# Kernel tuning notes

Hardware: AMD Instinct MI355X
Metric: run time of the kernel (lower is better)

The kernel has to match this reference:

```python
import jax, jax.numpy as jnp
import numpy as np

HEADS = 16
DIMS = [64, 64, 64, 64]  # [d_att(Q), d_att(K), d_ff(V), d_ff(G)]
EPS = 1e-4
P_POW = 2


def _cdist(Q, K):
    # Euclidean pairwise distance via the norm expansion, like torch.cdist.
    # Q: [h, b, t, d], K: [h, b, t, d] -> [h, b, t, t]
    q2 = jnp.sum(Q * Q, axis=-1)  # [h, b, t]
    k2 = jnp.sum(K * K, axis=-1)  # [h, b, t]
    qk = jnp.einsum('hbtd,hbsd->hbts', Q, K)
    d2 = q2[..., :, None] + k2[..., None, :] - 2.0 * qk
    return jnp.sqrt(jnp.maximum(d2, 0.0))


def setup_inputs() -> dict:
    key = jax.random.key(0)
    ks = jax.random.split(key, 4)
    b, t, d_in = 2, 2048, 1024
    d_proj = HEADS * sum(DIMS)  # 4096
    X = jax.random.normal(ks[0], (b, t, d_in), dtype=jnp.float32)
    W_in = jax.random.normal(ks[1], (d_in, d_proj), dtype=jnp.float32) * (d_in ** -0.5)
    b_in = jnp.zeros((d_proj,), dtype=jnp.float32)
    W_out = jax.random.normal(ks[2], (HEADS * DIMS[2], d_in), dtype=jnp.float32) * ((HEADS * DIMS[2]) ** -0.5)
    b_out = jnp.zeros((d_in,), dtype=jnp.float32)
    return {"X": X, "W_in": W_in, "b_in": b_in, "W_out": W_out, "b_out": b_out}


def reference(X, W_in, b_in, W_out, b_out):
    b, t, _ = X.shape
    # multi-head input projection: [b,t,d_in] -> [h,b,t,sum(DIMS)] -> split
    P = X @ W_in + b_in                       # [b, t, h*sum(DIMS)]
    P = P.reshape(b, t, HEADS, sum(DIMS))
    P = jnp.transpose(P, (2, 0, 1, 3))        # [h, b, t, sum(DIMS)]
    splits = np.cumsum(DIMS)[:-1]
    Q, K, V, G = jnp.split(P, splits, axis=-1)
    # Shepard's attention: inverse-power-distance weights
    W = jnp.power(EPS + _cdist(Q, K), -P_POW)         # [h, b, t, t]
    W = W / (EPS + jnp.sum(W, axis=-1, keepdims=True))
    A = jnp.einsum('hbts,hbse->hbte', W, V)           # [h, b, t, e]
    H = G * A                                          # gating
    H = jnp.transpose(H, (1, 2, 0, 3)).reshape(b, t, HEADS * DIMS[2])
    return H @ W_out + b_out
```

## Files before the change

### kernel.cpp

```cpp
#include <hip/hip_runtime.h>
#include <hip/hip_bf16.h>
#include <cstdint>
#include <cstddef>

typedef __bf16 bf16_t;
typedef __attribute__((ext_vector_type(8))) __bf16 bf16x8;
typedef __attribute__((ext_vector_type(4))) float f32x4;
typedef __attribute__((ext_vector_type(16))) float f32x16;
typedef __attribute__((ext_vector_type(4))) unsigned int u32x4;

#define ATT_EPS 1e-4f

__device__ __forceinline__ f32x4 mfma_bf16(bf16x8 a, bf16x8 b, f32x4 c) {
  return __builtin_amdgcn_mfma_f32_16x16x32_bf16(a, b, c, 0, 0, 0);
}
__device__ __forceinline__ f32x16 mfma32(bf16x8 a, bf16x8 b, f32x16 c) {
  return __builtin_amdgcn_mfma_f32_32x32x16_bf16(a, b, c, 0, 0, 0);
}
__device__ __forceinline__ unsigned cvtpk_bf16(float lo, float hi) {
  unsigned r;
  asm("v_cvt_pk_bf16_f32 %0, %1, %2" : "=v"(r) : "v"(lo), "v"(hi));
  return r;
}

#define GLDS16(g, l)                                                          \
  __builtin_amdgcn_global_load_lds(                                           \
      (const __attribute__((address_space(1))) void*)(g),                     \
      (__attribute__((address_space(3))) void*)(l), 16, 0, 0)

#define BARRAW() asm volatile("s_barrier" ::: "memory")
#define WAITVN(n) asm volatile("s_waitcnt vmcnt(" #n ")" ::: "memory")

__global__ __launch_bounds__(256) void prep_kernel(
    const float* __restrict__ Wi, bf16_t* __restrict__ WiT,
    const float* __restrict__ Wo, bf16_t* __restrict__ WoT,
    const float* __restrict__ X, bf16_t* __restrict__ Xb) {
  __shared__ float T[64][65];
  if (blockIdx.y >= 20) {
    int i = ((blockIdx.y - 20) * 64 + blockIdx.x) * 256 + threadIdx.x;
    const f32x4* src = (const f32x4*)X + (size_t)i * 4;
    f32x4 a = src[0], b = src[1], c = src[2], d = src[3];
    bf16x8 o0, o1;
    o0[0] = (__bf16)a[0]; o0[1] = (__bf16)a[1]; o0[2] = (__bf16)a[2]; o0[3] = (__bf16)a[3];
    o0[4] = (__bf16)b[0]; o0[5] = (__bf16)b[1]; o0[6] = (__bf16)b[2]; o0[7] = (__bf16)b[3];
    o1[0] = (__bf16)c[0]; o1[1] = (__bf16)c[1]; o1[2] = (__bf16)c[2]; o1[3] = (__bf16)c[3];
    o1[4] = (__bf16)d[0]; o1[5] = (__bf16)d[1]; o1[6] = (__bf16)d[2]; o1[7] = (__bf16)d[3];
    ((bf16x8*)Xb)[(size_t)i * 2] = o0;
    ((bf16x8*)Xb)[(size_t)i * 2 + 1] = o1;
    return;
  }
  int tx = threadIdx.x & 63, ty = threadIdx.x >> 6;
  const float* W;
  bf16_t* Wt;
  int c0, r0, R, C;
  if (blockIdx.y < 16) {
    W = Wi; Wt = WiT; R = 1024; C = 4096;
    c0 = blockIdx.x * 64; r0 = blockIdx.y * 64;
  } else {
    int idx = (blockIdx.y - 16) * 64 + blockIdx.x;
    if (idx >= 256) return;
    W = Wo; Wt = WoT; R = 1024; C = 1024;
    c0 = (idx & 15) * 64; r0 = (idx >> 4) * 64;
  }
#pragma unroll
  for (int i = 0; i < 16; ++i) {
    int rr = ty * 16 + i;
    T[rr][tx] = W[(size_t)(r0 + rr) * C + c0 + tx];
  }
  __syncthreads();
#pragma unroll
  for (int i = 0; i < 16; ++i) {
    int cc = ty * 16 + i;
    Wt[(size_t)(c0 + cc) * R + r0 + tx] = (bf16_t)T[tx][cc];
  }
}

__global__ __launch_bounds__(512, 2) void gemm1_kernel(
    const bf16_t* __restrict__ A, const bf16_t* __restrict__ Bt,
    const float* __restrict__ bias, bf16_t* __restrict__ P,
    float* __restrict__ Q2, bf16_t* __restrict__ K2E, bf16_t* __restrict__ VtG) {
  __shared__ bf16_t As[4][2][128 * 32];
  __shared__ bf16_t Bs[4][2][128 * 32];

  const int K = 1024, N = 4096;
  int tid = threadIdx.x, lane = tid & 63, wv = tid >> 6;
  int l15 = lane & 15, lhi = lane >> 4;
  int wm = wv >> 2, wn = wv & 3;
  int swz = (blockIdx.x & 7) * 32 + (blockIdx.x >> 3);
  int tm = swz >> 4, tn = swz & 15;
  int m0 = tm << 8, n0 = tn << 8;
  int h = tn;

  int srow = tid >> 2, su = tid & 3;
  int scc = (su ^ ((srow >> 1) & 3)) << 3;
  auto stage2 = [&](int t, int pq) {
    int k0 = t * 32 + scc;
    if (pq == 0) {
      GLDS16(A + (size_t)(m0 + srow) * K + k0, &As[t & 3][0][tid * 8]);
      GLDS16(A + (size_t)(m0 + 128 + srow) * K + k0, &As[t & 3][1][tid * 8]);
    } else {
      GLDS16(Bt + (size_t)(n0 + srow) * K + k0, &Bs[t & 3][0][tid * 8]);
      GLDS16(Bt + (size_t)(n0 + 128 + srow) * K + k0, &Bs[t & 3][1][tid * 8]);
    }
  };

  f32x4 zero = {0.f, 0.f, 0.f, 0.f};
  f32x4 acc[8][4];
#pragma unroll
  for (int mf = 0; mf < 8; ++mf)
#pragma unroll
    for (int nf = 0; nf < 4; ++nf) acc[mf][nf] = zero;

  int bh = wn >> 1;
  int cidb = (wn & 1) * 64 + l15;

  stage2(0, 0); stage2(0, 1);
  stage2(1, 0); stage2(1, 1);
  stage2(2, 0); stage2(2, 1);
  WAITVN(8);
  BARRAW();

  for (int t = 0; t < 32; ++t) {
    int buf = t & 3;
    bf16x8 af0[4], bfr[4];
#pragma unroll
    for (int i = 0; i < 4; ++i) {
      int mfr = i * 16 + l15;
      af0[i] = *(const bf16x8*)&As[buf][wm][mfr * 32 + ((lhi ^ ((mfr >> 1) & 3)) << 3)];
    }
#pragma unroll
    for (int nf = 0; nf < 4; ++nf) {
      int cid = cidb + nf * 16;
      bfr[nf] = *(const bf16x8*)&Bs[buf][bh][cid * 32 + ((lhi ^ ((cid >> 1) & 3)) << 3)];
    }
    if (t + 3 < 32) stage2(t + 3, 0);
#pragma unroll
    for (int i = 0; i < 4; ++i)
#pragma unroll
      for (int nf = 0; nf < 4; ++nf)
        acc[i][nf] = mfma_bf16(af0[i], bfr[nf], acc[i][nf]);
    bf16x8 af1[4];
#pragma unroll
    for (int i = 0; i < 4; ++i) {
      int mfr = (4 + i) * 16 + l15;
      af1[i] = *(const bf16x8*)&As[buf][wm][mfr * 32 + ((lhi ^ ((mfr >> 1) & 3)) << 3)];
    }
    if (t + 3 < 32) stage2(t + 3, 1);
#pragma unroll
    for (int i = 0; i < 4; ++i)
#pragma unroll
      for (int nf = 0; nf < 4; ++nf)
        acc[4 + i][nf] = mfma_bf16(af1[i], bfr[nf], acc[4 + i][nf]);
    if (t <= 28) WAITVN(8);
    else if (t == 29) WAITVN(4);
    else if (t == 30) WAITVN(0);
    BARRAW();
  }

#pragma unroll
  for (int nf = 0; nf < 4; ++nf) {
    float bv = bias[n0 + wn * 64 + nf * 16 + l15];
#pragma unroll
    for (int mf = 0; mf < 8; ++mf)
#pragma unroll
      for (int r = 0; r < 4; ++r) acc[mf][nf][r] += bv;
  }

  if (wn != 2) {
#pragma unroll
    for (int nf = 0; nf < 4; ++nf) {
      int col = n0 + wn * 64 + nf * 16 + l15;
#pragma unroll
      for (int mf = 0; mf < 8; ++mf) {
        int rowb = m0 + wm * 128 + mf * 16 + lhi * 4;
#pragma unroll
        for (int r = 0; r < 4; ++r)
          P[(size_t)(rowb + r) * N + col] = (bf16_t)acc[mf][nf][r];
      }
    }
  }

  if (wn < 2) {
#pragma unroll
    for (int mf = 0; mf < 8; ++mf)
#pragma unroll
      for (int r = 0; r < 4; ++r) {
        float s = 0.f;
#pragma unroll
        for (int nf = 0; nf < 4; ++nf) s += acc[mf][nf][r] * acc[mf][nf][r];
        s += __shfl_xor(s, 1);
        s += __shfl_xor(s, 2);
        s += __shfl_xor(s, 4);
        s += __shfl_xor(s, 8);
        if (l15 == 0) {
          int row = m0 + wm * 128 + mf * 16 + lhi * 4 + r;
          if (wn == 0) {
            Q2[h * 4096 + row] = s;
          } else {
            __bf16 kh = (__bf16)s;
            __bf16 kl = (__bf16)(s - (float)kh);
            bf16x8 rw;
            rw[0] = kh; rw[1] = kl;
            rw[2] = (__bf16)1.f; rw[3] = (__bf16)1.f;
            rw[4] = (__bf16)0.f; rw[5] = (__bf16)0.f;
            rw[6] = (__bf16)0.f; rw[7] = (__bf16)0.f;
            *(bf16x8*)&K2E[((size_t)h * 4096 + row) * 8] = rw;
          }
        }
      }
  }

  bf16_t* T = &As[0][0][0];
  if (wn == 2) {
#pragma unroll
    for (int mf = 0; mf < 8; ++mf)
#pragma unroll
      for (int nf = 0; nf < 4; ++nf)
#pragma unroll
        for (int r = 0; r < 4; ++r) {
          int row = wm * 128 + mf * 16 + lhi * 4 + r;
          int e = nf * 16 + l15;
          int prow = (row & ~15) | ((row & 3) | ((row & 4) << 1) | ((row & 8) >> 1));
          T[e * 264 + prow] = (bf16_t)acc[mf][nf][r];
        }
  }
  __syncthreads();
  {
    int e = tid >> 3, c0 = (tid & 7) * 32;
    bf16_t* dst = VtG + (size_t)(h * 64 + e) * 4096 + m0 + c0;
#pragma unroll
    for (int j = 0; j < 4; ++j)
      *(bf16x8*)&dst[j * 8] = *(bf16x8*)&T[e * 264 + c0 + j * 8];
  }
}

template <int OUTF32>
__global__ __launch_bounds__(256, 2) void gemm_kernel(
    const bf16_t* __restrict__ A, const bf16_t* __restrict__ Bt,
    const float* __restrict__ bias, void* __restrict__ Cout,
    int M, int N, int K) {
  __shared__ bf16_t As[2][128 * 64];
  __shared__ bf16_t Bs[2][128 * 64];
  int tid = threadIdx.x, lane = tid & 63, wv = tid >> 6;
  int l15 = lane & 15, lhi = lane >> 4;
  int NT = N >> 7;
  int nwg = gridDim.x;
  int qq = nwg >> 3;
  int swz = (blockIdx.x & 7) * qq + (blockIdx.x >> 3);
  int tm = swz / NT, tn = swz % NT;
  int m0 = tm << 7, n0 = tn << 7;
  int wm = (wv >> 1) << 6, wn = (wv & 1) << 6;
  int KT = K >> 6;

  auto stage = [&](int buf, int kt) {
    int k0 = kt << 6;
#pragma unroll
    for (int s = 0; s < 4; ++s) {
      int t = s * 256 + tid;
      int row = t >> 3, u = t & 7;
      int cc = (u ^ (row & 7)) << 3;
      GLDS16(A + (size_t)(m0 + row) * K + k0 + cc, &As[buf][t * 8]);
    }
#pragma unroll
    for (int s = 0; s < 4; ++s) {
      int t = s * 256 + tid;
      int row = t >> 3, u = t & 7;
      int cc = (u ^ (row & 7)) << 3;
      GLDS16(Bt + (size_t)(n0 + row) * K + k0 + cc, &Bs[buf][t * 8]);
    }
  };

  f32x4 zero = {0.f, 0.f, 0.f, 0.f};
  f32x4 acc[4][4];
#pragma unroll
  for (int ms = 0; ms < 4; ++ms)
#pragma unroll
    for (int ns = 0; ns < 4; ++ns) acc[ms][ns] = zero;

  stage(0, 0);
  __syncthreads();
  int cur = 0;
  for (int kt = 0; kt < KT; ++kt) {
    if (kt + 1 < KT) stage(cur ^ 1, kt + 1);
#pragma unroll
    for (int ks = 0; ks < 2; ++ks) {
      bf16x8 af[4], bfr[4];
#pragma unroll
      for (int ms = 0; ms < 4; ++ms) {
        int row = wm + ms * 16 + l15;
        af[ms] = *(const bf16x8*)&As[cur][row * 64 + (((ks * 4 + lhi) ^ (row & 7)) << 3)];
      }
#pragma unroll
      for (int ns = 0; ns < 4; ++ns) {
        int col = wn + ns * 16 + l15;
        bfr[ns] = *(const bf16x8*)&Bs[cur][col * 64 + (((ks * 4 + lhi) ^ (col & 7)) << 3)];
      }
#pragma unroll
      for (int ms = 0; ms < 4; ++ms)
#pragma unroll
        for (int ns = 0; ns < 4; ++ns)
          acc[ms][ns] = mfma_bf16(af[ms], bfr[ns], acc[ms][ns]);
    }
    __syncthreads();
    cur ^= 1;
  }

#pragma unroll
  for (int ns = 0; ns < 4; ++ns) {
    int col = n0 + wn + ns * 16 + l15;
    float bv = bias[col];
#pragma unroll
    for (int ms = 0; ms < 4; ++ms) {
      int rowb = m0 + wm + ms * 16 + lhi * 4;
#pragma unroll
      for (int r = 0; r < 4; ++r) {
        float v = acc[ms][ns][r] + bv;
        if (OUTF32)
          ((float*)Cout)[(size_t)(rowb + r) * N + col] = v;
        else
          ((bf16_t*)Cout)[(size_t)(rowb + r) * N + col] = (bf16_t)v;
      }
    }
  }
}

__global__ __launch_bounds__(512, 4) void attn_kernel(
    const bf16_t* __restrict__ P, const bf16_t* __restrict__ VtG,
    const float* __restrict__ Q2, const bf16_t* __restrict__ K2E,
    bf16_t* __restrict__ H) {
  __shared__ union Smem {
    struct {
      bf16_t Ks[2][64 * 64];
      bf16_t Vts[2][64 * 64];
      bf16_t K2e[2][64 * 8];
    } l;
    float Comb[4][64][33];
  } sm;
  __shared__ float invLds[4][32];

  int tid = threadIdx.x, lane = tid & 63, wv = tid >> 6;
  int l31 = lane & 31, hi = lane >> 5, hi4 = hi * 4;
  int qw = wv & 3, sw = wv >> 2;
  int sOff = sw * 32;
  int swz = (blockIdx.x & 7) * 64 + (blockIdx.x >> 3);
  int hb = swz >> 4, qt = swz & 15;
  int h = hb >> 1, b = hb & 1;
  int rowbase = b * 2048;
  const bf16_t* Pq = P + (size_t)rowbase * 4096 + h * 256;
  const bf16_t* Pk = Pq + 64;
  const bf16_t* Pg = Pq + 192;
  const bf16_t* Vg = VtG + (size_t)h * 64 * 4096 + rowbase;
  const float* Q2g = Q2 + h * 4096 + rowbase;
  const bf16_t* K2Eg = K2E + ((size_t)h * 4096 + rowbase) * 8;
  int q0 = qt * 128 + qw * 32;

  auto stageKV = [&](int buf, int s0) {
    {
      int row = tid >> 3, u = tid & 7;
      int cc = (u ^ (row & 7)) << 3;
      GLDS16(Pk + (size_t)(s0 + row) * 4096 + cc, &sm.l.Ks[buf][tid * 8]);
    }
    {
      int row = tid >> 3, u = tid & 7;
      int cc = (u ^ (row & 7)) << 3;
      GLDS16(Vg + (size_t)row * 4096 + s0 + cc, &sm.l.Vts[buf][tid * 8]);
    }
    if (tid < 64)
      GLDS16(K2Eg + (size_t)(s0 + tid) * 8, &sm.l.K2e[buf][tid * 8]);
  };

  bf16x8 qm[4];
#pragma unroll
  for (int db = 0; db < 4; ++db) {
    bf16x8 q = *(const bf16x8*)(Pq + (size_t)(q0 + l31) * 4096 + db * 16 + hi * 8);
    u32x4 u = *(u32x4*)&q;
    u = (u ^ 0x80008000u) + 0x00800080u;
    qm[db] = *(bf16x8*)&u;
  }
  float q2s = Q2g[q0 + l31];
  __bf16 q2h = (__bf16)q2s;
  __bf16 q2l = (__bf16)(q2s - (float)q2h);
  bf16x8 qmE;
  qmE[0] = hi ? (__bf16)0.f : (__bf16)1.f;
  qmE[1] = qmE[0];
  qmE[2] = hi ? (__bf16)0.f : q2h;
  qmE[3] = hi ? (__bf16)0.f : q2l;
  qmE[4] = (__bf16)0.f; qmE[5] = (__bf16)0.f;
  qmE[6] = (__bf16)0.f; qmE[7] = (__bf16)0.f;

  f32x16 zero16;
#pragma unroll
  for (int r = 0; r < 16; ++r) zero16[r] = 0.f;

  f32x16 nacc0 = zero16, nacc1 = zero16;
  float dacc0 = 0.f, dacc1 = 0.f;

  stageKV(0, 0);
  __syncthreads();

  for (int st = 0; st < 32; ++st) {
    int cur = st & 1;
    int s0 = st * 64;
    if (st + 1 < 32) stageKV(cur ^ 1, s0 + 64);

    const bf16_t* KsC = sm.l.Ks[cur];
    const bf16_t* VtC = sm.l.Vts[cur];
    const bf16_t* K2eC = sm.l.K2e[cur];
    {
      int srow = sOff + l31;
      bf16x8 ke = *(const bf16x8*)&K2eC[srow * 8];
      u32x4 keu = *(u32x4*)&ke;
      u32x4 kz;
      kz[0] = hi ? 0u : keu[0];
      kz[1] = hi ? 0u : keu[1];
      kz[2] = 0u; kz[3] = 0u;
      bf16x8 kfE = *(bf16x8*)&kz;
      f32x16 D = mfma32(kfE, qmE, zero16);
#pragma unroll
      for (int db = 0; db < 4; ++db) {
        bf16x8 kf = *(const bf16x8*)&KsC[srow * 64 + (((db * 2 + hi) ^ (srow & 7)) << 3)];
        D = mfma32(kf, qm[db], D);
      }
      float p[16];
#pragma unroll
      for (int r = 0; r < 16; ++r) {
        float w = __builtin_amdgcn_rcpf(fmaxf(D[r], 1e-12f));
        if (r & 1) dacc1 += w; else dacc0 += w;
        p[r] = w;
      }
      u32x4 w0v = {cvtpk_bf16(p[0], p[1]), cvtpk_bf16(p[2], p[3]),
                   cvtpk_bf16(p[4], p[5]), cvtpk_bf16(p[6], p[7])};
      u32x4 w1v = {cvtpk_bf16(p[8], p[9]), cvtpk_bf16(p[10], p[11]),
                   cvtpk_bf16(p[12], p[13]), cvtpk_bf16(p[14], p[15])};
      bf16x8 pa0 = *(bf16x8*)&w0v;
      bf16x8 pa1 = *(bf16x8*)&w1v;
      int e = l31;
      int ciB = sw * 4;
      bf16x8 vb00 = *(const bf16x8*)&VtC[e * 64 + (((ciB + 0 + hi) ^ (e & 7)) << 3)];
      bf16x8 vb01 = *(const bf16x8*)&VtC[(e + 32) * 64 + (((ciB + 0 + hi) ^ ((e + 32) & 7)) << 3)];
      bf16x8 vb10 = *(const bf16x8*)&VtC[e * 64 + (((ciB + 2 + hi) ^ (e & 7)) << 3)];
      bf16x8 vb11 = *(const bf16x8*)&VtC[(e + 32) * 64 + (((ciB + 2 + hi) ^ ((e + 32) & 7)) << 3)];
      nacc0 = mfma32(pa0, vb00, nacc0);
      nacc1 = mfma32(pa0, vb01, nacc1);
      nacc0 = mfma32(pa1, vb10, nacc0);
      nacc1 = mfma32(pa1, vb11, nacc1);
    }
    __syncthreads();
  }

  if (sw == 1) {
#pragma unroll
    for (int r = 0; r < 16; ++r) {
      sm.Comb[qw][lane][r] = nacc0[r];
      sm.Comb[qw][lane][16 + r] = nacc1[r];
    }
    sm.Comb[qw][lane][32] = dacc0 + dacc1;
  }
  __syncthreads();
  if (sw == 0) {
    float dacc = dacc0 + dacc1 + sm.Comb[qw][lane][32];
#pragma unroll
    for (int r = 0; r < 16; ++r) {
      nacc0[r] += sm.Comb[qw][lane][r];
      nacc1[r] += sm.Comb[qw][lane][16 + r];
    }
    dacc += __shfl_xor(dacc, 32);
    float inv = __builtin_amdgcn_rcpf(ATT_EPS + dacc);
    if (lane < 32) invLds[qw][l31] = inv;
    __builtin_amdgcn_s_waitcnt(0);
#pragma unroll
    for (int r = 0; r < 16; ++r) {
      int q = (r & 3) + 8 * (r >> 2) + hi4;
      int tq = q0 + q;
      float iv = invLds[qw][q];
      float g0 = (float)Pg[(size_t)tq * 4096 + l31];
      float g1 = (float)Pg[(size_t)tq * 4096 + 32 + l31];
      H[(size_t)(rowbase + tq) * 1024 + h * 64 + l31] = (bf16_t)(g0 * nacc0[r] * iv);
      H[(size_t)(rowbase + tq) * 1024 + h * 64 + 32 + l31] = (bf16_t)(g1 * nacc1[r] * iv);
    }
  }
}

extern "C" void kernel_launch(void* const* d_in, const int* in_sizes, int n_in,
                              void* d_out, int out_size, void* d_ws, size_t ws_size,
                              hipStream_t stream) {
  const float* X     = (const float*)d_in[0];
  const float* W_in  = (const float*)d_in[1];
  const float* b_in  = (const float*)d_in[2];
  const float* W_out = (const float*)d_in[3];
  const float* b_out = (const float*)d_in[4];

  char* ws = (char*)d_ws;
  bf16_t* Xb  = (bf16_t*)(ws);
  bf16_t* WbT = (bf16_t*)(ws + ((size_t)8  << 20));
  bf16_t* WoT = (bf16_t*)(ws + ((size_t)16 << 20));
  bf16_t* Pb  = (bf16_t*)(ws + ((size_t)18 << 20));
  bf16_t* Hb  = (bf16_t*)(ws + ((size_t)50 << 20));
  float*  Q2  = (float*) (ws + ((size_t)58 << 20));
  bf16_t* VtG = (bf16_t*)d_out;
  bf16_t* K2E = (bf16_t*)((char*)d_out + ((size_t)8 << 20));

  prep_kernel<<<dim3(64, 36), 256, 0, stream>>>(W_in, WbT, W_out, WoT, X, Xb);
  gemm1_kernel<<<256, 512, 0, stream>>>(Xb, WbT, b_in, Pb, Q2, K2E, VtG);
  attn_kernel<<<512, 512, 0, stream>>>(Pb, VtG, Q2, K2E, Hb);
  gemm_kernel<1><<<256, 256, 0, stream>>>(Hb, WoT, b_out, d_out, 4096, 1024, 1024);
}
```

Baseline: 127.4 us.

## Quad-buffer K/V tiles and process two key tiles per barrier

Grows the shared-memory K/V staging from two buffers to four and restructures the key loop to handle two 64-key tiles per barrier phase. Both QK distance MFMA chains are issued before the two PV updates, which adds instruction-level parallelism, and the number of __syncthreads is halved. The cost is roughly double the LDS per block, which may cut how many blocks can be resident per CU under the existing launch bounds, and more live registers.

```diff
diff --git a/kernel.cpp b/kernel.cpp
--- a/kernel.cpp
+++ b/kernel.cpp
@@ -330,9 +330,9 @@
     bf16_t* __restrict__ H) {
   __shared__ union Smem {
     struct {
-      bf16_t Ks[2][64 * 64];
-      bf16_t Vts[2][64 * 64];
-      bf16_t K2e[2][64 * 8];
+      bf16_t Ks[4][64 * 64];
+      bf16_t Vts[4][64 * 64];
+      bf16_t K2e[4][64 * 8];
     } l;
     float Comb[4][64][33];
   } sm;
@@ -395,57 +395,73 @@
   f32x16 nacc0 = zero16, nacc1 = zero16;
   float dacc0 = 0.f, dacc1 = 0.f;
 
+  auto qkD = [&](const bf16_t* KsC, const bf16_t* K2eC) -> f32x16 {
+    int srow = sOff + l31;
+    bf16x8 ke = *(const bf16x8*)&K2eC[srow * 8];
+    u32x4 keu = *(u32x4*)&ke;
+    u32x4 kz;
+    kz[0] = hi ? 0u : keu[0];
+    kz[1] = hi ? 0u : keu[1];
+    kz[2] = 0u; kz[3] = 0u;
+    bf16x8 kfE = *(bf16x8*)&kz;
+    f32x16 D = mfma32(kfE, qmE, zero16);
+#pragma unroll
+    for (int db = 0; db < 4; ++db) {
+      bf16x8 kf = *(const bf16x8*)&KsC[srow * 64 + (((db * 2 + hi) ^ (srow & 7)) << 3)];
+      D = mfma32(kf, qm[db], D);
+    }
+    return D;
+  };
+  auto pv = [&](f32x16 D, const bf16_t* VtC) {
+    float p[16];
+#pragma unroll
+    for (int r = 0; r < 16; ++r) {
+      float w = __builtin_amdgcn_rcpf(fmaxf(D[r], 1e-12f));
+      if (r & 1) dacc1 += w; else dacc0 += w;
+      p[r] = w;
+    }
+    u32x4 w0v = {cvtpk_bf16(p[0], p[1]), cvtpk_bf16(p[2], p[3]),
+                 cvtpk_bf16(p[4], p[5]), cvtpk_bf16(p[6], p[7])};
+    u32x4 w1v = {cvtpk_bf16(p[8], p[9]), cvtpk_bf16(p[10], p[11]),
+                 cvtpk_bf16(p[12], p[13]), cvtpk_bf16(p[14], p[15])};
+    bf16x8 pa0 = *(bf16x8*)&w0v;
+    bf16x8 pa1 = *(bf16x8*)&w1v;
+    int e = l31;
+    int ciB = sw * 4;
+    bf16x8 vb00 = *(const bf16x8*)&VtC[e * 64 + (((ciB + 0 + hi) ^ (e & 7)) << 3)];
+    bf16x8 vb01 = *(const bf16x8*)&VtC[(e + 32) * 64 + (((ciB + 0 + hi) ^ ((e + 32) & 7)) << 3)];
+    bf16x8 vb10 = *(const bf16x8*)&VtC[e * 64 + (((ciB + 2 + hi) ^ (e & 7)) << 3)];
+    bf16x8 vb11 = *(const bf16x8*)&VtC[(e + 32) * 64 + (((ciB + 2 + hi) ^ ((e + 32) & 7)) << 3)];
+    nacc0 = mfma32(pa0, vb00, nacc0);
+    nacc1 = mfma32(pa0, vb01, nacc1);
+    nacc0 = mfma32(pa1, vb10, nacc0);
+    nacc1 = mfma32(pa1, vb11, nacc1);
+  };
+
   stageKV(0, 0);
+  stageKV(1, 64);
+  stageKV(2, 128);
+  stageKV(3, 192);
   __syncthreads();
 
-  for (int st = 0; st < 32; ++st) {
-    int cur = st & 1;
-    int s0 = st * 64;
-    if (st + 1 < 32) stageKV(cur ^ 1, s0 + 64);
-
-    const bf16_t* KsC = sm.l.Ks[cur];
-    const bf16_t* VtC = sm.l.Vts[cur];
-    const bf16_t* K2eC = sm.l.K2e[cur];
+  for (int m = 0; m < 8; ++m) {
+    int s0 = m * 256;
     {
-      int srow = sOff + l31;
-      bf16x8 ke = *(const bf16x8*)&K2eC[srow * 8];
-      u32x4 keu = *(u32x4*)&ke;
-      u32x4 kz;
-      kz[0] = hi ? 0u : keu[0];
-      kz[1] = hi ? 0u : keu[1];
-      kz[2] = 0u; kz[3] = 0u;
-      bf16x8 kfE = *(bf16x8*)&kz;
-      f32x16 D = mfma32(kfE, qmE, zero16);
-#pragma unroll
-      for (int db = 0; db < 4; ++db) {
-        bf16x8 kf = *(const bf16x8*)&KsC[srow * 64 + (((db * 2 + hi) ^ (srow & 7)) << 3)];
-        D = mfma32(kf, qm[db], D);
-      }
-      float p[16];
-#pragma unroll
-      for (int r = 0; r < 16; ++r) {
-        float w = __builtin_amdgcn_rcpf(fmaxf(D[r], 1e-12f));
-        if (r & 1) dacc1 += w; else dacc0 += w;
-        p[r] = w;
-      }
-      u32x4 w0v = {cvtpk_bf16(p[0], p[1]), cvtpk_bf16(p[2], p[3]),
-                   cvtpk_bf16(p[4], p[5]), cvtpk_bf16(p[6], p[7])};
-      u32x4 w1v = {cvtpk_bf16(p[8], p[9]), cvtpk_bf16(p[10], p[11]),
-                   cvtpk_bf16(p[12], p[13]), cvtpk_bf16(p[14], p[15])};
-      bf16x8 pa0 = *(bf16x8*)&w0v;
-      bf16x8 pa1 = *(bf16x8*)&w1v;
-      int e = l31;
-      int ciB = sw * 4;
-      bf16x8 vb00 = *(const bf16x8*)&VtC[e * 64 + (((ciB + 0 + hi) ^ (e & 7)) << 3)];
-      bf16x8 vb01 = *(const bf16x8*)&VtC[(e + 32) * 64 + (((ciB + 0 + hi) ^ ((e + 32) & 7)) << 3)];
-      bf16x8 vb10 = *(const bf16x8*)&VtC[e * 64 + (((ciB + 2 + hi) ^ (e & 7)) << 3)];
-      bf16x8 vb11 = *(const bf16x8*)&VtC[(e + 32) * 64 + (((ciB + 2 + hi) ^ ((e + 32) & 7)) << 3)];
-      nacc0 = mfma32(pa0, vb00, nacc0);
-      nacc1 = mfma32(pa0, vb01, nacc1);
-      nacc0 = mfma32(pa1, vb10, nacc0);
-      nacc1 = mfma32(pa1, vb11, nacc1);
-    }
-    __syncthreads();
+      if (m > 0) { stageKV(2, s0 + 128); stageKV(3, s0 + 192); }
+      f32x16 Da = qkD(sm.l.Ks[0], sm.l.K2e[0]);
+      f32x16 Db = qkD(sm.l.Ks[1], sm.l.K2e[1]);
+      pv(Da, sm.l.Vts[0]);
+      pv(Db, sm.l.Vts[1]);
+      __syncthreads();
+    }
+    {
+      if (m < 7) { stageKV(0, s0 + 256); stageKV(1, s0 + 320); }
+      f32x16 Da = qkD(sm.l.Ks[2], sm.l.K2e[2]);
+      f32x16 Db = qkD(sm.l.Ks[3], sm.l.K2e[3]);
+      pv(Da, sm.l.Vts[2]);
+      pv(Db, sm.l.Vts[3]);
+      __syncthreads();
+    }
   }
 
   if (sw == 1) {
```

Measured after the change: 145.1 us. 13.9% more time.
